# Performance work log

Hardware: AMD Instinct MI355X
Metric: run time of the kernel (lower is better)

Reference implementation:

```python
import jax, jax.numpy as jnp
import numpy as np

BS, Z, NOBJ = 16384, 512, 64


def setup_inputs() -> dict:
    key = jax.random.key(0)
    ks = jax.random.split(key, 12)
    din = Z + 4  # z concatenated with bounds (x_size = 0)

    def lin(k, i, o):
        kw, kb = jax.random.split(k)
        w = jax.random.normal(kw, (i, o), jnp.float32) * (1.0 / np.sqrt(i))
        b = jax.random.normal(kb, (o,), jnp.float32) * 0.01
        return w, b

    W1, c1 = lin(ks[0], din, 512)
    W2, c2 = lin(ks[1], 512, 256)
    W3, c3 = lin(ks[2], 256, 128)
    W4, c4 = lin(ks[3], 128, 64)
    W5, c5 = lin(ks[4], 64, NOBJ * 4)
    z = jax.random.normal(ks[5], (BS, Z), jnp.float32)
    # room bounds [x_min, y_min, x_max, y_max]; must allow gaps >= 1
    bounds = jnp.array([0.0, 0.0, 40.0, 40.0], jnp.float32)
    return {"z": z, "bounds": bounds,
            "W1": W1, "c1": c1, "W2": W2, "c2": c2, "W3": W3, "c3": c3,
            "W4": W4, "c4": c4, "W5": W5, "c5": c5}


def _lrelu(v):
    return jnp.where(v > 0, v, 0.2 * v)


def _solve_axis(pp, pg, lo, hi):
    """Exact KKT solution of: min (x-pp)^2 + (g-pg)^2  s.t. x>=lo, g>=1, x+g<=hi.
    Returns (x, w) with w = x + g. Matches the parabolic QP per object/axis."""
    x0 = jnp.maximum(pp, lo)          # box projection (lower bounds only)
    g0 = jnp.maximum(pg, 1.0)
    t = 0.5 * (hi - pp - pg)          # projection of (pp,pg) onto line x+g=hi
    xl = jnp.clip(pp + t, lo, hi - 1.0)
    over = (x0 + g0) > hi             # coupling constraint active?
    x = jnp.where(over, xl, x0)
    g = jnp.where(over, hi - xl, g0)
    return x, x + g


def reference(z, bounds, W1, c1, W2, c2, W3, c3, W4, c4, W5, c5):
    bs = z.shape[0]
    bnd = jnp.broadcast_to(bounds, (bs, 4))
    h = jnp.concatenate([z, bnd], axis=1)          # (bs, z_size+4)
    h = _lrelu(h @ W1 + c1)                        # dropout treated as eval/identity
    h = _lrelu(h @ W2 + c2)
    h = _lrelu(h @ W3 + c3)
    h = _lrelu(h @ W4 + c4)
    p = (h @ W5 + c5).reshape(bs, NOBJ, 4)         # per-object params [px, py, pw, ph]
    px, py, pw, ph = p[..., 0], p[..., 1], p[..., 2], p[..., 3]
    b0, b1, b2, b3 = bounds[0], bounds[1], bounds[2], bounds[3]
    # QP objective: sum (x-px)^2+(y-py)^2+((w-x)-pw)^2+((h-y)-ph)^2
    # s.t. x>=b0, y>=b1, w<=b2, h<=b3, x<=w-1, y<=h-1. Separable per object/axis.
    xs, ws = _solve_axis(px, pw, b0, b2)
    ys, hs = _solve_axis(py, ph, b1, b3)
    return jnp.stack([xs, ys, ws, hs], axis=-1)    # (bs, num_objs, 4)
```

## Files before the change

kernel.cpp:

```cpp
#include <hip/hip_runtime.h>


#define MROWS 16384

typedef __attribute__((ext_vector_type(8))) short bf16x8;
typedef __attribute__((ext_vector_type(4))) float floatx4;

__device__ __forceinline__ unsigned short f2bf(float x) {
    union { float f; unsigned u; } c; c.f = x;
    unsigned r = c.u + 0x7fffu + ((c.u >> 16) & 1u);
    return (unsigned short)(r >> 16);
}
__device__ __forceinline__ float bf2f(unsigned short b) {
    union { unsigned u; float f; } c; c.u = ((unsigned)b) << 16;
    return c.f;
}

__device__ __forceinline__ bf16x8 gload(const unsigned short* p) {
    bf16x8 r;
    asm volatile("global_load_dwordx4 %0, %1, off"
                 : "=&v"(r)
                 : "v"((unsigned long long)(size_t)p)
                 : "memory");
    return r;
}
template<int IMM>
__device__ __forceinline__ void vwait(bf16x8& v) {
    asm volatile("s_waitcnt vmcnt(%1)" : "+v"(v) : "n"(IMM) : "memory");
}
__device__ __forceinline__ void drain8(bf16x8 (&r)[8]) {
    asm volatile("s_waitcnt vmcnt(0)"
                 : "+v"(r[0]), "+v"(r[1]), "+v"(r[2]), "+v"(r[3]),
                   "+v"(r[4]), "+v"(r[5]), "+v"(r[6]), "+v"(r[7])
                 :: "memory");
}
__device__ __forceinline__ void drain4(bf16x8 (&r)[4]) {
    asm volatile("s_waitcnt vmcnt(0)"
                 : "+v"(r[0]), "+v"(r[1]), "+v"(r[2]), "+v"(r[3])
                 :: "memory");
}

__global__ __launch_bounds__(256) void pack_wt(
    const float* __restrict__ W1, unsigned short* __restrict__ T1,
    const float* __restrict__ W2, unsigned short* __restrict__ T2,
    const float* __restrict__ W3, unsigned short* __restrict__ T3,
    const float* __restrict__ W4, unsigned short* __restrict__ T4,
    const float* __restrict__ W5, unsigned short* __restrict__ T5)
{
    const int idx = blockIdx.x * 256 + threadIdx.x;
    if (blockIdx.y == 4) {
        if (idx >= 256 * 64) return;
        const int k = idx >> 8, n = idx & 255;
        const float v = W5[idx];
        const unsigned short hi = f2bf(v);
        const unsigned short lo = f2bf(v - bf2f(hi));
        const int ntile = n >> 4, m_l = n & 15;
        const int ks = k >> 5, quad = (k >> 3) & 3, e = k & 7;
        const size_t b = (size_t)(((ks * 16 + ntile) * 2) * 64 + quad * 16 + m_l) * 8 + e;
        T5[b] = hi; T5[b + 512] = lo;
        return;
    }
    const float* W; unsigned short* T; int Kreal, nshift;
    switch (blockIdx.y) {
        case 0:  W = W1; T = T1; Kreal = 516; nshift = 9; break;
        case 1:  W = W2; T = T2; Kreal = 512; nshift = 8; break;
        case 2:  W = W3; T = T3; Kreal = 256; nshift = 7; break;
        default: W = W4; T = T4; Kreal = 128; nshift = 6; break;
    }
    const int N = 1 << nshift, NT = N >> 4;
    const int KS = (Kreal + 31) >> 5;
    if (idx >= N * KS * 32) return;
    const int k = idx >> nshift;
    const int n = idx & (N - 1);
    const unsigned short v = (k < Kreal) ? f2bf(W[idx]) : (unsigned short)0;
    const int ntile = n >> 4, m_l = n & 15;
    const int ks = k >> 5, quad = (k >> 3) & 3, e = k & 7;
    T[(size_t)((ks * NT + ntile) * 64 + quad * 16 + m_l) * 8 + e] = v;
}

#define OFF_ZS   0
#define LD_ZS    552
#define OFF_H1   17664
#define LD_H1    520
#define OFF_H2   0
#define LD_H2    264
#define OFF_H3   17664
#define LD_H3    136
#define OFF_H4   8448
#define LD_H4    72
#define OFF_P    17664
#define LD_P     260
#define LDS_TOT  34304

template<int NF, int KSTEPS, int NT, int DEP>
__device__ __forceinline__ void layer_stream(
    unsigned short* lds, int offA, int lda, int offC, int ldc,
    const unsigned short* __restrict__ Wt,
    const float* __restrict__ bias, int wid, int lane)
{
    const int m_l = lane & 15, quad = lane >> 4;
    constexpr int NFR = NF * KSTEPS;
    const unsigned short* __restrict__ Wb = Wt + ((size_t)(wid * NF) * 64 + lane) * 8;

    floatx4 acc[2][NF];
    #pragma unroll
    for (int j = 0; j < NF; ++j) {
        const float bv = bias[wid * (NF * 16) + j * 16 + m_l];
        acc[0][j] = (floatx4){bv, bv, bv, bv};
        acc[1][j] = (floatx4){bv, bv, bv, bv};
    }

    bf16x8 ring[DEP];
    #pragma unroll
    for (int f = 0; f < DEP; ++f) {
        const int g = (f < NFR) ? f : 0;
        ring[f] = gload(Wb + (size_t)((g / NF) * NT + (g % NF)) * 512);
    }
    bf16x8 a0, a1;
    #pragma unroll
    for (int f = 0; f < NFR; ++f) {
        const int ks = f / NF, j = f - ks * NF;
        if (j == 0) {
            a0 = *(const bf16x8*)&lds[offA + (m_l     ) * lda + ks*32 + quad*8];
            a1 = *(const bf16x8*)&lds[offA + (m_l + 16) * lda + ks*32 + quad*8];
        }
        vwait<DEP - 1>(ring[f % DEP]);
        acc[0][j] = __builtin_amdgcn_mfma_f32_16x16x32_bf16(a0, ring[f % DEP], acc[0][j], 0, 0, 0);
        acc[1][j] = __builtin_amdgcn_mfma_f32_16x16x32_bf16(a1, ring[f % DEP], acc[1][j], 0, 0, 0);
        const int nf2 = (f + DEP < NFR) ? f + DEP : 0;
        ring[f % DEP] = gload(Wb + (size_t)((nf2 / NF) * NT + (nf2 % NF)) * 512);
    }
    if constexpr (DEP == 8) drain8(ring); else drain4(ring);

    #pragma unroll
    for (int j = 0; j < NF; ++j) {
        const int col = wid * (NF * 16) + j * 16 + m_l;
        #pragma unroll
        for (int i = 0; i < 2; ++i)
            #pragma unroll
            for (int r = 0; r < 4; ++r) {
                float v = acc[i][j][r];
                v = v > 0.f ? v : 0.2f * v;
                lds[offC + (i*16 + quad*4 + r) * ldc + col] = f2bf(v);
            }
    }
}

__global__ __launch_bounds__(256, 2) void fused_mlp_qp(
    const float* __restrict__ z, const float* __restrict__ bounds,
    const unsigned short* __restrict__ Wt1, const float* __restrict__ c1,
    const unsigned short* __restrict__ Wt2, const float* __restrict__ c2,
    const unsigned short* __restrict__ Wt3, const float* __restrict__ c3,
    const unsigned short* __restrict__ Wt4, const float* __restrict__ c4,
    const unsigned short* __restrict__ Wt5, const float* __restrict__ c5,
    float* __restrict__ out)
{
    __shared__ unsigned short lds[LDS_TOT];
    const int tid  = threadIdx.x;
    const int wid  = tid >> 6, lane = tid & 63;
    const int m_l  = lane & 15, quad = lane >> 4;
    const int bm   = blockIdx.x * 32;

    const float4 bnd = *(const float4*)bounds;

    {
        const float4* __restrict__ zf = (const float4*)(z + (size_t)bm * 512);
        #pragma unroll
        for (int i = 0; i < 16; ++i) {
            const int f   = i * 256 + tid;
            const int row = f >> 7, c4i = f & 127;
            const float4 v = zf[f];
            unsigned short t4[4] = {f2bf(v.x), f2bf(v.y), f2bf(v.z), f2bf(v.w)};
            *(uint2*)&lds[OFF_ZS + row * LD_ZS + c4i * 4] = *(uint2*)t4;
        }
        if (tid < 160) {
            const int row = tid / 5, j = tid % 5;
            unsigned short t8[8] = {0,0,0,0,0,0,0,0};
            if (j == 0) { t8[0] = f2bf(bnd.x); t8[1] = f2bf(bnd.y);
                          t8[2] = f2bf(bnd.z); t8[3] = f2bf(bnd.w); }
            *(uint4*)&lds[OFF_ZS + row * LD_ZS + 512 + j * 8] = *(uint4*)t8;
        }
    }
    __syncthreads();

    layer_stream<8,17,32,8>(lds, OFF_ZS, LD_ZS, OFF_H1, LD_H1, Wt1, c1, wid, lane);
    __syncthreads();
    layer_stream<4,16,16,8>(lds, OFF_H1, LD_H1, OFF_H2, LD_H2, Wt2, c2, wid, lane);
    __syncthreads();
    layer_stream<2,8, 8, 8>(lds, OFF_H2, LD_H2, OFF_H3, LD_H3, Wt3, c3, wid, lane);
    __syncthreads();
    layer_stream<1,4, 4, 4>(lds, OFF_H3, LD_H3, OFF_H4, LD_H4, Wt4, c4, wid, lane);
    __syncthreads();

    {
        const unsigned short* __restrict__ Wb5 = Wt5 + (size_t)wid * 4096 + (size_t)lane * 8;
        floatx4 acc[2][4];
        #pragma unroll
        for (int j = 0; j < 4; ++j) {
            const float bv = c5[wid * 64 + j * 16 + m_l];
            acc[0][j] = (floatx4){bv, bv, bv, bv};
            acc[1][j] = (floatx4){bv, bv, bv, bv};
        }
        auto w5off = [](int g) {
            const int ks = g >> 3, rem = g & 7;
            return (size_t)ks * 16384 + (size_t)(rem >> 1) * 1024 + (size_t)(rem & 1) * 512;
        };
        bf16x8 ring[8];
        #pragma unroll
        for (int f = 0; f < 8; ++f) ring[f] = gload(Wb5 + w5off(f));
        bf16x8 a0, a1;
        #pragma unroll
        for (int f = 0; f < 16; ++f) {
            const int ks = f >> 3, rem = f & 7, j = rem >> 1;
            if (rem == 0) {
                a0 = *(const bf16x8*)&lds[OFF_H4 + (m_l     ) * LD_H4 + ks*32 + quad*8];
                a1 = *(const bf16x8*)&lds[OFF_H4 + (m_l + 16) * LD_H4 + ks*32 + quad*8];
            }
            vwait<7>(ring[f & 7]);
            acc[0][j] = __builtin_amdgcn_mfma_f32_16x16x32_bf16(a0, ring[f & 7], acc[0][j], 0, 0, 0);
            acc[1][j] = __builtin_amdgcn_mfma_f32_16x16x32_bf16(a1, ring[f & 7], acc[1][j], 0, 0, 0);
            const int nf2 = (f + 8 < 16) ? f + 8 : 0;
            ring[f & 7] = gload(Wb5 + w5off(nf2));
        }
        drain8(ring);

        float* __restrict__ p = (float*)&lds[OFF_P];
        #pragma unroll
        for (int j = 0; j < 4; ++j) {
            const int col = wid * 64 + j * 16 + m_l;
            #pragma unroll
            for (int i = 0; i < 2; ++i)
                #pragma unroll
                for (int r = 0; r < 4; ++r)
                    p[(i*16 + quad*4 + r) * LD_P + col] = acc[i][j][r];
        }
    }
    __syncthreads();

    const float b0 = bnd.x, b1 = bnd.y, b2 = bnd.z, b3 = bnd.w;
    const float* __restrict__ p = (const float*)&lds[OFF_P];
    #pragma unroll
    for (int i = 0; i < 8; ++i) {
        const int row = i * 4 + wid;
        const float4 pv = *(const float4*)&p[row * LD_P + lane * 4];
        float xs, wo, ys, ho;
        {
            const float px = pv.x, pw = pv.z;
            const float x0 = fmaxf(px, b0);
            const float g0 = fmaxf(pw, 1.0f);
            const float t  = 0.5f * (b2 - px - pw);
            const float xl = fminf(fmaxf(px + t, b0), b2 - 1.0f);
            const bool over = (x0 + g0) > b2;
            const float x = over ? xl : x0;
            const float g = over ? (b2 - xl) : g0;
            xs = x; wo = x + g;
        }
        {
            const float py = pv.y, ph = pv.w;
            const float x0 = fmaxf(py, b1);
            const float g0 = fmaxf(ph, 1.0f);
            const float t  = 0.5f * (b3 - py - ph);
            const float xl = fminf(fmaxf(py + t, b1), b3 - 1.0f);
            const bool over = (x0 + g0) > b3;
            const float x = over ? xl : x0;
            const float g = over ? (b3 - xl) : g0;
            ys = x; ho = x + g;
        }
        float4 o; o.x = xs; o.y = ys; o.z = wo; o.w = ho;
        ((float4*)out)[(size_t)(bm + row) * 64 + lane] = o;
    }
}

extern "C" void kernel_launch(void* const* d_in, const int* in_sizes, int n_in,
                              void* d_out, int out_size, void* d_ws, size_t ws_size,
                              hipStream_t stream) {
    const float* z      = (const float*)d_in[0];
    const float* bounds = (const float*)d_in[1];
    const float* W1 = (const float*)d_in[2];
    const float* c1 = (const float*)d_in[3];
    const float* W2 = (const float*)d_in[4];
    const float* c2 = (const float*)d_in[5];
    const float* W3 = (const float*)d_in[6];
    const float* c3 = (const float*)d_in[7];
    const float* W4 = (const float*)d_in[8];
    const float* c4 = (const float*)d_in[9];
    const float* W5 = (const float*)d_in[10];
    const float* c5 = (const float*)d_in[11];
    float* out = (float*)d_out;

    unsigned short* ws  = (unsigned short*)d_ws;
    unsigned short* Wt1 = ws;
    unsigned short* Wt2 = Wt1 + 278528;
    unsigned short* Wt3 = Wt2 + 131072;
    unsigned short* Wt4 = Wt3 + 32768;
    unsigned short* Wt5 = Wt4 + 8192;

    pack_wt<<<dim3(1088, 5), 256, 0, stream>>>(
        W1, Wt1, W2, Wt2, W3, Wt3, W4, Wt4, W5, Wt5);
    fused_mlp_qp<<<dim3(MROWS / 32), 256, 0, stream>>>(
        z, bounds, Wt1, c1, Wt2, c2, Wt3, c3, Wt4, c4, Wt5, c5, out);
}
```

Measured before the change: 124.3 us.

## Process 64 rows per block with 8 waves and deepen weight prefetch ring

Doubles the block to 512 threads and 64 rows, with two wave-rows each handling 32 rows against the same weight column slices. This lets weight tiles be fetched once per block for twice as many rows, so global weight traffic per row drops. The prefetch ring depth also grows from 8 to 16 for the larger layers. The cost is double the LDS (about 137 KB per block) and more VGPRs, which lowers occupancy, and at 256 blocks there is only about one block per CU.

```diff
diff --git a/kernel.cpp b/kernel.cpp
--- a/kernel.cpp
+++ b/kernel.cpp
@@ -28,16 +28,16 @@
 __device__ __forceinline__ void vwait(bf16x8& v) {
     asm volatile("s_waitcnt vmcnt(%1)" : "+v"(v) : "n"(IMM) : "memory");
 }
-__device__ __forceinline__ void drain8(bf16x8 (&r)[8]) {
+__device__ __forceinline__ void drain4(bf16x8 (&r)[4]) {
+    asm volatile("s_waitcnt vmcnt(0)"
+                 : "+v"(r[0]), "+v"(r[1]), "+v"(r[2]), "+v"(r[3]) :: "memory");
+}
+__device__ __forceinline__ void drain16(bf16x8 (&r)[16]) {
     asm volatile("s_waitcnt vmcnt(0)"
                  : "+v"(r[0]), "+v"(r[1]), "+v"(r[2]), "+v"(r[3]),
-                   "+v"(r[4]), "+v"(r[5]), "+v"(r[6]), "+v"(r[7])
-                 :: "memory");
-}
-__device__ __forceinline__ void drain4(bf16x8 (&r)[4]) {
-    asm volatile("s_waitcnt vmcnt(0)"
-                 : "+v"(r[0]), "+v"(r[1]), "+v"(r[2]), "+v"(r[3])
-                 :: "memory");
+                   "+v"(r[4]), "+v"(r[5]), "+v"(r[6]), "+v"(r[7]),
+                   "+v"(r[8]), "+v"(r[9]), "+v"(r[10]), "+v"(r[11]),
+                   "+v"(r[12]), "+v"(r[13]), "+v"(r[14]), "+v"(r[15]) :: "memory");
 }
 
 __global__ __launch_bounds__(256) void pack_wt(
@@ -80,32 +80,32 @@
 
 #define OFF_ZS   0
 #define LD_ZS    552
-#define OFF_H1   17664
+#define OFF_H1   35328
 #define LD_H1    520
 #define OFF_H2   0
 #define LD_H2    264
-#define OFF_H3   17664
+#define OFF_H3   35328
 #define LD_H3    136
-#define OFF_H4   8448
+#define OFF_H4   44032
 #define LD_H4    72
-#define OFF_P    17664
+#define OFF_P    0
 #define LD_P     260
-#define LDS_TOT  34304
+#define LDS_TOT  68608
 
 template<int NF, int KSTEPS, int NT, int DEP>
 __device__ __forceinline__ void layer_stream(
     unsigned short* lds, int offA, int lda, int offC, int ldc,
     const unsigned short* __restrict__ Wt,
-    const float* __restrict__ bias, int wid, int lane)
+    const float* __restrict__ bias, int wn, int mrow, int lane)
 {
     const int m_l = lane & 15, quad = lane >> 4;
     constexpr int NFR = NF * KSTEPS;
-    const unsigned short* __restrict__ Wb = Wt + ((size_t)(wid * NF) * 64 + lane) * 8;
+    const unsigned short* __restrict__ Wb = Wt + ((size_t)(wn * NF) * 64 + lane) * 8;
 
     floatx4 acc[2][NF];
     #pragma unroll
     for (int j = 0; j < NF; ++j) {
-        const float bv = bias[wid * (NF * 16) + j * 16 + m_l];
+        const float bv = bias[wn * (NF * 16) + j * 16 + m_l];
         acc[0][j] = (floatx4){bv, bv, bv, bv};
         acc[1][j] = (floatx4){bv, bv, bv, bv};
     }
@@ -121,8 +121,8 @@
     for (int f = 0; f < NFR; ++f) {
         const int ks = f / NF, j = f - ks * NF;
         if (j == 0) {
-            a0 = *(const bf16x8*)&lds[offA + (m_l     ) * lda + ks*32 + quad*8];
-            a1 = *(const bf16x8*)&lds[offA + (m_l + 16) * lda + ks*32 + quad*8];
+            a0 = *(const bf16x8*)&lds[offA + (mrow + m_l     ) * lda + ks*32 + quad*8];
+            a1 = *(const bf16x8*)&lds[offA + (mrow + m_l + 16) * lda + ks*32 + quad*8];
         }
         vwait<DEP - 1>(ring[f % DEP]);
         acc[0][j] = __builtin_amdgcn_mfma_f32_16x16x32_bf16(a0, ring[f % DEP], acc[0][j], 0, 0, 0);
@@ -130,23 +130,23 @@
         const int nf2 = (f + DEP < NFR) ? f + DEP : 0;
         ring[f % DEP] = gload(Wb + (size_t)((nf2 / NF) * NT + (nf2 % NF)) * 512);
     }
-    if constexpr (DEP == 8) drain8(ring); else drain4(ring);
+    if constexpr (DEP == 16) drain16(ring); else drain4(ring);
 
     #pragma unroll
     for (int j = 0; j < NF; ++j) {
-        const int col = wid * (NF * 16) + j * 16 + m_l;
+        const int col = wn * (NF * 16) + j * 16 + m_l;
         #pragma unroll
         for (int i = 0; i < 2; ++i)
             #pragma unroll
             for (int r = 0; r < 4; ++r) {
                 float v = acc[i][j][r];
                 v = v > 0.f ? v : 0.2f * v;
-                lds[offC + (i*16 + quad*4 + r) * ldc + col] = f2bf(v);
+                lds[offC + (mrow + i*16 + quad*4 + r) * ldc + col] = f2bf(v);
             }
     }
 }
 
-__global__ __launch_bounds__(256, 2) void fused_mlp_qp(
+__global__ __launch_bounds__(512, 2) void fused_mlp_qp(
     const float* __restrict__ z, const float* __restrict__ bounds,
     const unsigned short* __restrict__ Wt1, const float* __restrict__ c1,
     const unsigned short* __restrict__ Wt2, const float* __restrict__ c2,
@@ -158,8 +158,10 @@
     __shared__ unsigned short lds[LDS_TOT];
     const int tid  = threadIdx.x;
     const int wid  = tid >> 6, lane = tid & 63;
+    const int wm   = wid >> 2, wn = wid & 3;
+    const int mrow = wm * 32;
     const int m_l  = lane & 15, quad = lane >> 4;
-    const int bm   = blockIdx.x * 32;
+    const int bm   = blockIdx.x * 64;
 
     const float4 bnd = *(const float4*)bounds;
 
@@ -167,13 +169,13 @@
         const float4* __restrict__ zf = (const float4*)(z + (size_t)bm * 512);
         #pragma unroll
         for (int i = 0; i < 16; ++i) {
-            const int f   = i * 256 + tid;
+            const int f   = i * 512 + tid;
             const int row = f >> 7, c4i = f & 127;
             const float4 v = zf[f];
             unsigned short t4[4] = {f2bf(v.x), f2bf(v.y), f2bf(v.z), f2bf(v.w)};
             *(uint2*)&lds[OFF_ZS + row * LD_ZS + c4i * 4] = *(uint2*)t4;
         }
-        if (tid < 160) {
+        if (tid < 320) {
             const int row = tid / 5, j = tid % 5;
             unsigned short t8[8] = {0,0,0,0,0,0,0,0};
             if (j == 0) { t8[0] = f2bf(bnd.x); t8[1] = f2bf(bnd.y);
@@ -183,21 +185,21 @@
     }
     __syncthreads();
 
-    layer_stream<8,17,32,8>(lds, OFF_ZS, LD_ZS, OFF_H1, LD_H1, Wt1, c1, wid, lane);
-    __syncthreads();
-    layer_stream<4,16,16,8>(lds, OFF_H1, LD_H1, OFF_H2, LD_H2, Wt2, c2, wid, lane);
-    __syncthreads();
-    layer_stream<2,8, 8, 8>(lds, OFF_H2, LD_H2, OFF_H3, LD_H3, Wt3, c3, wid, lane);
-    __syncthreads();
-    layer_stream<1,4, 4, 4>(lds, OFF_H3, LD_H3, OFF_H4, LD_H4, Wt4, c4, wid, lane);
+    layer_stream<8,17,32,16>(lds, OFF_ZS, LD_ZS, OFF_H1, LD_H1, Wt1, c1, wn, mrow, lane);
+    __syncthreads();
+    layer_stream<4,16,16,16>(lds, OFF_H1, LD_H1, OFF_H2, LD_H2, Wt2, c2, wn, mrow, lane);
+    __syncthreads();
+    layer_stream<2,8, 8, 16>(lds, OFF_H2, LD_H2, OFF_H3, LD_H3, Wt3, c3, wn, mrow, lane);
+    __syncthreads();
+    layer_stream<1,4, 4, 4 >(lds, OFF_H3, LD_H3, OFF_H4, LD_H4, Wt4, c4, wn, mrow, lane);
     __syncthreads();
 
     {
-        const unsigned short* __restrict__ Wb5 = Wt5 + (size_t)wid * 4096 + (size_t)lane * 8;
+        const unsigned short* __restrict__ Wb5 = Wt5 + (size_t)wn * 4096 + (size_t)lane * 8;
         floatx4 acc[2][4];
         #pragma unroll
         for (int j = 0; j < 4; ++j) {
-            const float bv = c5[wid * 64 + j * 16 + m_l];
+            const float bv = c5[wn * 64 + j * 16 + m_l];
             acc[0][j] = (floatx4){bv, bv, bv, bv};
             acc[1][j] = (floatx4){bv, bv, bv, bv};
         }
@@ -205,34 +207,33 @@
             const int ks = g >> 3, rem = g & 7;
             return (size_t)ks * 16384 + (size_t)(rem >> 1) * 1024 + (size_t)(rem & 1) * 512;
         };
-        bf16x8 ring[8];
-        #pragma unroll
-        for (int f = 0; f < 8; ++f) ring[f] = gload(Wb5 + w5off(f));
+        bf16x8 ring[16];
+        #pragma unroll
+        for (int f = 0; f < 16; ++f) ring[f] = gload(Wb5 + w5off(f));
         bf16x8 a0, a1;
         #pragma unroll
         for (int f = 0; f < 16; ++f) {
             const int ks = f >> 3, rem = f & 7, j = rem >> 1;
             if (rem == 0) {
-                a0 = *(const bf16x8*)&lds[OFF_H4 + (m_l     ) * LD_H4 + ks*32 + quad*8];
-                a1 = *(const bf16x8*)&lds[OFF_H4 + (m_l + 16) * LD_H4 + ks*32 + quad*8];
+                a0 = *(const bf16x8*)&lds[OFF_H4 + (mrow + m_l     ) * LD_H4 + ks*32 + quad*8];
+                a1 = *(const bf16x8*)&lds[OFF_H4 + (mrow + m_l + 16) * LD_H4 + ks*32 + quad*8];
             }
-            vwait<7>(ring[f & 7]);
-            acc[0][j] = __builtin_amdgcn_mfma_f32_16x16x32_bf16(a0, ring[f & 7], acc[0][j], 0, 0, 0);
-            acc[1][j] = __builtin_amdgcn_mfma_f32_16x16x32_bf16(a1, ring[f & 7], acc[1][j], 0, 0, 0);
-            const int nf2 = (f + 8 < 16) ? f + 8 : 0;
-            ring[f & 7] = gload(Wb5 + w5off(nf2));
-        }
-        drain8(ring);
+            vwait<15>(ring[f]);
+            acc[0][j] = __builtin_amdgcn_mfma_f32_16x16x32_bf16(a0, ring[f], acc[0][j], 0, 0, 0);
+            acc[1][j] = __builtin_amdgcn_mfma_f32_16x16x32_bf16(a1, ring[f], acc[1][j], 0, 0, 0);
+            ring[f] = gload(Wb5 + w5off(0));
+        }
+        drain16(ring);
 
         float* __restrict__ p = (float*)&lds[OFF_P];
         #pragma unroll
         for (int j = 0; j < 4; ++j) {
-            const int col = wid * 64 + j * 16 + m_l;
+            const int col = wn * 64 + j * 16 + m_l;
             #pragma unroll
             for (int i = 0; i < 2; ++i)
                 #pragma unroll
                 for (int r = 0; r < 4; ++r)
-                    p[(i*16 + quad*4 + r) * LD_P + col] = acc[i][j][r];
+                    p[(mrow + i*16 + quad*4 + r) * LD_P + col] = acc[i][j][r];
         }
     }
     __syncthreads();
@@ -241,7 +242,7 @@
     const float* __restrict__ p = (const float*)&lds[OFF_P];
     #pragma unroll
     for (int i = 0; i < 8; ++i) {
-        const int row = i * 4 + wid;
+        const int row = i * 8 + wid;
         const float4 pv = *(const float4*)&p[row * LD_P + lane * 4];
         float xs, wo, ys, ho;
         {
@@ -297,6 +298,6 @@
 
     pack_wt<<<dim3(1088, 5), 256, 0, stream>>>(
         W1, Wt1, W2, Wt2, W3, Wt3, W4, Wt4, W5, Wt5);
-    fused_mlp_qp<<<dim3(MROWS / 32), 256, 0, stream>>>(
+    fused_mlp_qp<<<dim3(MROWS / 64), 512, 0, stream>>>(
         z, bounds, Wt1, c1, Wt2, c2, Wt3, c3, Wt4, c4, Wt5, c5, out);
 }
```

After: 127.6 us. 2.6% more time.
